# Performance work log

Measured on AMD Instinct MI355X. Metric: run time of the kernel, lower is better.

## Reference

```python
import jax, jax.numpy as jnp
import numpy as np


def setup_inputs() -> dict:
    key = jax.random.key(0)
    k1, k2 = jax.random.split(key)
    data = jax.random.normal(k1, (16, 64, 128, 128), dtype=jnp.float32)
    weights = jax.random.normal(k2, (128, 64, 3, 3), dtype=jnp.float32)
    return {"data": data, "weights": weights}


def reference(data, weights):
    # Original module performs im2col (unfold+reshape) + matmul, which is
    # mathematically a stride-1 VALID cross-correlation in NCHW layout.
    # weights: [C_out, C_in, kH, kW]; output: [B, C_out, H-kH+1, W-kW+1]
    return jax.lax.conv_general_dilated(
        data, weights,
        window_strides=(1, 1),
        padding="VALID",
        dimension_numbers=("NCHW", "OIHW", "NCHW"),
    )
```

## Files before the change

kernel.cpp:

```cpp
#include <hip/hip_runtime.h>


#define BATCH 16
#define CIN   64
#define HIN   128
#define WIN   128
#define COUT  128
#define HO    126
#define WO    126

typedef short bf16x8 __attribute__((ext_vector_type(8)));
typedef float f32x4  __attribute__((ext_vector_type(4)));
typedef float f32x2  __attribute__((ext_vector_type(2)));

__device__ __forceinline__ unsigned short f2bf(float f) {
    union { float f; unsigned int u; } v; v.f = f;
    unsigned int u = v.u;
    unsigned int r = (u + 0x7fffu + ((u >> 16) & 1u)) >> 16;
    return (unsigned short)r;
}

__device__ __forceinline__ void async16(const void* g, void* l) {
    __builtin_amdgcn_global_load_lds(
        (const __attribute__((address_space(1))) unsigned int*)(unsigned long long)g,
        (__attribute__((address_space(3))) unsigned int*)(unsigned long long)l,
        16, 0, 0);
}

__global__ __launch_bounds__(256) void t1_nchw_to_nhwc(
        const float* __restrict__ x, unsigned short* __restrict__ y) {
    __shared__ unsigned short tile[64 * 68];
    const int b = blockIdx.z, h = blockIdx.y, w0 = blockIdx.x * 64;
    const int t = threadIdx.x;

    const int wl = t & 63, ci0 = t >> 6;
    const float* src = x + (((size_t)b * CIN) * HIN + h) * WIN + w0 + wl;
#pragma unroll
    for (int j = 0; j < 16; j++) {
        const int ci = ci0 + j * 4;
        tile[wl * 68 + ci] = f2bf(src[(size_t)ci * (HIN * WIN)]);
    }
    __syncthreads();

    const int ci4 = (t & 15) * 4, wl2 = t >> 4;
#pragma unroll
    for (int j = 0; j < 4; j++) {
        const int w = wl2 + j * 16;
        ushort4 v = *(const ushort4*)&tile[w * 68 + ci4];
        *(ushort4*)&y[(((size_t)b * HIN + h) * WIN + w0 + w) * CIN + ci4] = v;
    }
}

__global__ __launch_bounds__(256) void t2_weights(
        const float* __restrict__ w, unsigned short* __restrict__ wt) {
    const int idx = blockIdx.x * 256 + threadIdx.x;
    if (idx < COUT * CIN * 9) {
        const int co = idx / (CIN * 9);
        const int r  = idx % (CIN * 9);
        const int ci = r / 9;
        const int k  = r % 9;
        wt[((size_t)k * COUT + co) * CIN + ci] = f2bf(w[idx]);
    }
}

__global__ __launch_bounds__(256, 2) void conv_mfma(
        const unsigned short* __restrict__ nhwc,
        const unsigned short* __restrict__ wt,
        float* __restrict__ out) {
    __shared__ __align__(16) char smem[49408];
    short* Bs = (short*)smem;
    float* Cb = (float*)smem;

    const int raw = blockIdx.y * 126 + blockIdx.x;
    const int s = (raw & 7) * 252 + (raw >> 3);
    const int b = s / 126;
    const int oh = s - b * 126;

    const int tid = threadIdx.x;
    const int lane = tid & 63, wave = tid >> 6;
    const int wm = wave & 1, wn = wave >> 1;
    const int col = lane & 15, quad = lane >> 4;
    const int swl = (lane * 16) ^ ((lane >> 3) << 4);

    {
        const char* src = (const char*)nhwc + (size_t)(b * HIN + oh) * (WIN * CIN * 2);
        char* dst = (char*)Bs;
#pragma unroll
        for (int i = 0; i < 12; i++) {
            const int c = wave * 12 + i;
            async16(src + c * 1024 + swl, dst + c * 1024 + lane * 16);
        }
    }

    const unsigned short* wbase = wt + (size_t)(wm * 64 + col) * CIN + quad * 8;

#define LOADA(dst, t) do {                                                   \
    _Pragma("unroll") for (int mi_ = 0; mi_ < 4; mi_++)                      \
    _Pragma("unroll") for (int kk_ = 0; kk_ < 2; kk_++)                      \
        dst[mi_][kk_] = *(const bf16x8*)(wbase +                             \
            ((t) * COUT + mi_ * 16) * CIN + kk_ * 32);                       \
} while (0)

    bf16x8 aA[4][2], aB[4][2];
    LOADA(aA, 0);

    __syncthreads();

    f32x4 acc[4][4] = {};

#pragma unroll
    for (int t = 0; t < 9; t++) {
        const int kh = t / 3, kw = t - kh * 3;
        if (t + 1 < 9) {
            if (t & 1) LOADA(aA, t + 1); else LOADA(aB, t + 1);
        }
#pragma unroll
        for (int kk = 0; kk < 2; kk++) {
            bf16x8 bb[4];
#pragma unroll
            for (int ni = 0; ni < 4; ni++) {
                const int r = kh * 128 + wn * 64 + ni * 16 + col + kw;
                bb[ni] = *(const bf16x8*)&Bs[(r * 64 + kk * 32 + quad * 8) ^ ((r & 7) << 3)];
            }
#pragma unroll
            for (int mi = 0; mi < 4; mi++)
#pragma unroll
                for (int ni = 0; ni < 4; ni++)
                    acc[mi][ni] = __builtin_amdgcn_mfma_f32_16x16x32_bf16(
                        (t & 1) ? aB[mi][kk] : aA[mi][kk], bb[ni], acc[mi][ni], 0, 0, 0);
        }
    }

#pragma unroll
    for (int h = 0; h < 2; h++) {
        __syncthreads();
        if (wm == h) {
#pragma unroll
            for (int mi = 0; mi < 4; mi++)
#pragma unroll
                for (int ni = 0; ni < 4; ni++) {
                    const int n = wn * 64 + ni * 16 + col;
#pragma unroll
                    for (int r = 0; r < 4; r++)
                        Cb[(mi * 16 + quad * 4 + r) * 130 + n] = acc[mi][ni][r];
                }
        }
        __syncthreads();
        if (lane < 63) {
#pragma unroll
            for (int j = 0; j < 16; j++) {
                const int cp = wave * 16 + j;
                f32x2 v = *(const f32x2*)&Cb[cp * 130 + lane * 2];
                float* o = out + (((size_t)b * COUT + h * 64 + cp) * HO + oh) * WO + lane * 2;
                *(f32x2*)o = v;
            }
        }
    }
}

__global__ __launch_bounds__(256) void conv_direct(
        const float* __restrict__ x, const float* __restrict__ w,
        float* __restrict__ y) {
    const int idx = blockIdx.x * 256 + threadIdx.x;
    if (idx >= BATCH * COUT * HO * WO) return;
    const int ow = idx % WO;
    int t = idx / WO;
    const int oh = t % HO; t /= HO;
    const int co = t % COUT;
    const int b  = t / COUT;
    float acc = 0.f;
    const float* xb = x + (((size_t)b * CIN) * HIN + oh) * WIN + ow;
    const float* wc = w + (size_t)co * (CIN * 9);
    for (int ci = 0; ci < CIN; ci++) {
#pragma unroll
        for (int kh = 0; kh < 3; kh++)
#pragma unroll
            for (int kw = 0; kw < 3; kw++)
                acc += xb[(size_t)ci * (HIN * WIN) + kh * WIN + kw] * wc[ci * 9 + kh * 3 + kw];
    }
    y[idx] = acc;
}

extern "C" void kernel_launch(void* const* d_in, const int* in_sizes, int n_in,
                              void* d_out, int out_size, void* d_ws, size_t ws_size,
                              hipStream_t stream) {
    const float* data    = (const float*)d_in[0];
    const float* weights = (const float*)d_in[1];
    float* out = (float*)d_out;

    const size_t nhwc_bytes = (size_t)BATCH * HIN * WIN * CIN * 2;
    const size_t slack = 4096;
    const size_t wt_bytes = (size_t)9 * COUT * CIN * 2;
    const size_t need = nhwc_bytes + slack + wt_bytes;

    if (ws_size >= need) {
        unsigned short* nhwc = (unsigned short*)d_ws;
        unsigned short* wt   = (unsigned short*)((char*)d_ws + nhwc_bytes + slack);
        t1_nchw_to_nhwc<<<dim3(2, HIN, BATCH), 256, 0, stream>>>(data, nhwc);
        t2_weights<<<(COUT * CIN * 9 + 255) / 256, 256, 0, stream>>>(weights, wt);
        conv_mfma<<<dim3(126, BATCH), 256, 0, stream>>>(nhwc, wt, out);
    } else {
        const int n = BATCH * COUT * HO * WO;
        conv_direct<<<(n + 255) / 256, 256, 0, stream>>>(data, weights, out);
    }
}
```

Baseline: 264.2 us.

## Stage conv weights in LDS with async double buffering on 512-thread blocks

Weights for each filter tap are now copied asynchronously into a double-buffered, swizzled LDS region, replacing the per-thread global register loads. The block grows to 8 waves, each computing a 32-channel by 64-pixel tile, which halves the accumulator registers per thread. The LDS-staged transpose epilogue is replaced by direct per-lane global stores. The intent is less global weight traffic and more waves in flight, at the cost of a barrier after every tap and less coalesced output writes.

Measured after the change: 244.6 us. 7.4% less time.

```diff
diff --git a/kernel.cpp b/kernel.cpp
--- a/kernel.cpp
+++ b/kernel.cpp
@@ -11,7 +11,6 @@
 
 typedef short bf16x8 __attribute__((ext_vector_type(8)));
 typedef float f32x4  __attribute__((ext_vector_type(4)));
-typedef float f32x2  __attribute__((ext_vector_type(2)));
 
 __device__ __forceinline__ unsigned short f2bf(float f) {
     union { float f; unsigned int u; } v; v.f = f;
@@ -63,96 +62,98 @@
     }
 }
 
-__global__ __launch_bounds__(256, 2) void conv_mfma(
+__global__ __launch_bounds__(512, 2) void conv_mfma(
         const unsigned short* __restrict__ nhwc,
         const unsigned short* __restrict__ wt,
         float* __restrict__ out) {
-    __shared__ __align__(16) char smem[49408];
+    __shared__ __align__(16) char smem[49408 + 32768];
     short* Bs = (short*)smem;
-    float* Cb = (float*)smem;
+    short* As = (short*)(smem + 49408);
 
     const int raw = blockIdx.y * 126 + blockIdx.x;
     const int s = (raw & 7) * 252 + (raw >> 3);
     const int b = s / 126;
     const int oh = s - b * 126;
 
-    const int tid = threadIdx.x;
-    const int lane = tid & 63, wave = tid >> 6;
-    const int wm = wave & 1, wn = wave >> 1;
-    const int col = lane & 15, quad = lane >> 4;
+    const int tid  = threadIdx.x;
+    const int lane = tid & 63, wid = tid >> 6;
+    const int co0  = (wid & 3) * 32;
+    const int wn   = wid >> 1 & 0;
+    const int spn  = wid >> 2;
+    const int col  = lane & 15, quad = lane >> 4;
     const int swl = (lane * 16) ^ ((lane >> 3) << 4);
 
     {
         const char* src = (const char*)nhwc + (size_t)(b * HIN + oh) * (WIN * CIN * 2);
         char* dst = (char*)Bs;
 #pragma unroll
-        for (int i = 0; i < 12; i++) {
-            const int c = wave * 12 + i;
+        for (int i = 0; i < 6; i++) {
+            const int c = wid * 6 + i;
             async16(src + c * 1024 + swl, dst + c * 1024 + lane * 16);
         }
     }
-
-    const unsigned short* wbase = wt + (size_t)(wm * 64 + col) * CIN + quad * 8;
-
-#define LOADA(dst, t) do {                                                   \
-    _Pragma("unroll") for (int mi_ = 0; mi_ < 4; mi_++)                      \
-    _Pragma("unroll") for (int kk_ = 0; kk_ < 2; kk_++)                      \
-        dst[mi_][kk_] = *(const bf16x8*)(wbase +                             \
-            ((t) * COUT + mi_ * 16) * CIN + kk_ * 32);                       \
-} while (0)
-
-    bf16x8 aA[4][2], aB[4][2];
-    LOADA(aA, 0);
-
+    {
+        const char* srcA = (const char*)wt;
+        char* dstA = (char*)As;
+#pragma unroll
+        for (int i = 0; i < 2; i++) {
+            const int c = wid * 2 + i;
+            async16(srcA + c * 1024 + swl, dstA + c * 1024 + lane * 16);
+        }
+    }
     __syncthreads();
 
-    f32x4 acc[4][4] = {};
+    f32x4 acc[2][4] = {};
 
 #pragma unroll
     for (int t = 0; t < 9; t++) {
         const int kh = t / 3, kw = t - kh * 3;
+
         if (t + 1 < 9) {
-            if (t & 1) LOADA(aA, t + 1); else LOADA(aB, t + 1);
-        }
+            const char* srcA = (const char*)wt + (size_t)(t + 1) * 16384;
+            char* dstA = (char*)As + ((t + 1) & 1) * 16384;
+#pragma unroll
+            for (int i = 0; i < 2; i++) {
+                const int c = wid * 2 + i;
+                async16(srcA + c * 1024 + swl, dstA + c * 1024 + lane * 16);
+            }
+        }
+
+        const short* At = As + (t & 1) * 8192;
 #pragma unroll
         for (int kk = 0; kk < 2; kk++) {
-            bf16x8 bb[4];
+            bf16x8 aa[2], bb[4];
+#pragma unroll
+            for (int mi = 0; mi < 2; mi++) {
+                const int r = co0 + mi * 16 + col;
+                aa[mi] = *(const bf16x8*)&At[(r * 64 + kk * 32 + quad * 8) ^ ((r & 7) << 3)];
+            }
 #pragma unroll
             for (int ni = 0; ni < 4; ni++) {
-                const int r = kh * 128 + wn * 64 + ni * 16 + col + kw;
+                const int r = kh * 128 + spn * 64 + ni * 16 + col + kw;
                 bb[ni] = *(const bf16x8*)&Bs[(r * 64 + kk * 32 + quad * 8) ^ ((r & 7) << 3)];
             }
 #pragma unroll
-            for (int mi = 0; mi < 4; mi++)
+            for (int mi = 0; mi < 2; mi++)
 #pragma unroll
                 for (int ni = 0; ni < 4; ni++)
                     acc[mi][ni] = __builtin_amdgcn_mfma_f32_16x16x32_bf16(
-                        (t & 1) ? aB[mi][kk] : aA[mi][kk], bb[ni], acc[mi][ni], 0, 0, 0);
-        }
-    }
-
-#pragma unroll
-    for (int h = 0; h < 2; h++) {
-        __syncthreads();
-        if (wm == h) {
-#pragma unroll
-            for (int mi = 0; mi < 4; mi++)
-#pragma unroll
-                for (int ni = 0; ni < 4; ni++) {
-                    const int n = wn * 64 + ni * 16 + col;
-#pragma unroll
-                    for (int r = 0; r < 4; r++)
-                        Cb[(mi * 16 + quad * 4 + r) * 130 + n] = acc[mi][ni][r];
-                }
-        }
-        __syncthreads();
-        if (lane < 63) {
-#pragma unroll
-            for (int j = 0; j < 16; j++) {
-                const int cp = wave * 16 + j;
-                f32x2 v = *(const f32x2*)&Cb[cp * 130 + lane * 2];
-                float* o = out + (((size_t)b * COUT + h * 64 + cp) * HO + oh) * WO + lane * 2;
-                *(f32x2*)o = v;
+                        aa[mi], bb[ni], acc[mi][ni], 0, 0, 0);
+        }
+        if (t + 1 < 9) __syncthreads();
+    }
+
+#pragma unroll
+    for (int ni = 0; ni < 4; ni++) {
+        const int ow = spn * 64 + ni * 16 + col;
+        if (ow < WO) {
+#pragma unroll
+            for (int mi = 0; mi < 2; mi++) {
+                const int co = co0 + mi * 16 + quad * 4;
+                float* o = out + (((size_t)b * COUT + co) * HO + oh) * WO + ow;
+#pragma unroll
+                for (int r = 0; r < 4; r++)
+                    o[(size_t)r * HO * WO] = acc[mi][ni][r];
             }
         }
     }
@@ -198,7 +199,7 @@
         unsigned short* wt   = (unsigned short*)((char*)d_ws + nhwc_bytes + slack);
         t1_nchw_to_nhwc<<<dim3(2, HIN, BATCH), 256, 0, stream>>>(data, nhwc);
         t2_weights<<<(COUT * CIN * 9 + 255) / 256, 256, 0, stream>>>(weights, wt);
-        conv_mfma<<<dim3(126, BATCH), 256, 0, stream>>>(nhwc, wt, out);
+        conv_mfma<<<dim3(126, BATCH), 512, 0, stream>>>(nhwc, wt, out);
     } else {
         const int n = BATCH * COUT * HO * WO;
         conv_direct<<<(n + 255) / 256, 256, 0, stream>>>(data, weights, out);
```
